# Kernel optimization log

Hardware: AMD Instinct MI355X
Metric: run time of the kernel (lower is better)

The kernel has to match this reference:

```python
import jax, jax.numpy as jnp
import numpy as np

LEVELS = 256
# round(d*cos(a)), round(d*sin(a)) for d=1, angles 0, pi/4, pi/2, 3pi/4 (torch defaults)
SHIFTS = [(1, 0), (1, 1), (0, 1), (-1, 1)]


def _glcm(gray):
    # gray: (n, h, w) int32 in [0, LEVELS-1]
    n = gray.shape[0]
    B = LEVELS * LEVELS
    cooc = []
    for dx, dy in SHIFTS:  # fixed small set of angles
        shifted = jnp.roll(gray, shift=(dx, dy), axis=(1, 2))
        joint = (gray * LEVELS + shifted).reshape(n, -1)  # (n, h*w)
        vmin = joint.min()
        vmax = joint.max()
        # faithful torch.histc binning: B equal-width bins over [vmin, vmax],
        # values == vmax fall in last bin (handled by clip)
        scale = B / jnp.maximum((vmax - vmin).astype(jnp.float32), 1.0)
        bins = jnp.clip(
            jnp.floor((joint - vmin).astype(jnp.float32) * scale).astype(jnp.int32),
            0, B - 1)
        bidx = jnp.broadcast_to(jnp.arange(n)[:, None], joint.shape)
        hist = jnp.zeros((n, B), jnp.float32).at[bidx, bins].add(1.0)
        cooc.append(hist.reshape(n, LEVELS, LEVELS).sum(axis=0))
    co = jnp.stack(cooc, axis=-1)            # (L, L, A)
    co = co + jnp.swapaxes(co, 0, 1)          # symmetric=True
    glcm = co / co.sum()                      # normalize over ALL dims incl. angles (as torch)
    return glcm[:, :, None, :]                # (L, L, n_dist=1, A)


def _contrast(glcm):
    i = jnp.arange(LEVELS, dtype=jnp.float32)
    w = (i[:, None] - i[None, :]) ** 2        # (L, L) contrast weights
    return jnp.sum(glcm * w[:, :, None, None], axis=(0, 1))  # (n_dist, A)


def _loss(original, generated):
    og = jax.lax.stop_gradient(
        jnp.round(original.mean(axis=1) * (LEVELS - 1)).astype(jnp.int32))
    gg = jax.lax.stop_gradient(
        jnp.round(generated.mean(axis=1) * (LEVELS - 1)).astype(jnp.int32))
    return jnp.mean(jnp.abs(_contrast(_glcm(og)) - _contrast(_glcm(gg))))


def setup_inputs() -> dict:
    key = jax.random.key(0)
    k1, k2 = jax.random.split(key)
    shape = (16, 3, 512, 512)
    return {
        "original": jax.random.uniform(k1, shape, dtype=jnp.float32),
        "generated": jax.random.uniform(k2, shape, dtype=jnp.float32),
    }


def reference(original, generated):
    return _loss(original, generated)
```

## Files before the change

kernel.cpp:

```cpp
#include <hip/hip_runtime.h>

#define W 512
#define NPIX 4194304

union Bytes { uint4 v; unsigned char b[16]; };

__device__ __forceinline__ unsigned char gray1(float a, float b, float c) {
    return (unsigned char)__float2int_rn(((a + b + c) / 3.0f) * 255.0f);
}

__global__ __launch_bounds__(256, 4) void k1_gray_minmax(
    const float4* __restrict__ og, const float4* __restrict__ gg,
    uchar4* __restrict__ gray, unsigned int* __restrict__ blockmm) {
    int inp = blockIdx.y;
    int img = blockIdx.x >> 5;
    int r0 = (blockIdx.x & 31) << 4;
    const float4* src = (inp ? gg : og) + (size_t)img * 3 * 65536;
    uchar4* gout = gray + (size_t)inp * (NPIX / 4) + img * 65536;
    const float4* s0 = src;
    const float4* s1 = src + 65536;
    const float4* s2 = src + 131072;

    __shared__ unsigned char lds[18 * W];
    uchar4* lds4 = (uchar4*)lds;

    int off[9];
#pragma unroll
    for (int j = 0; j < 9; ++j) {
        int q = threadIdx.x + j * 256;
        int i = q >> 7, quad = q & 127;
        int ir = (r0 - 1 + i) & 511;
        off[j] = ir * 128 + quad;
    }
    float4 a = s0[off[0]], b = s1[off[0]], c = s2[off[0]];
#pragma unroll
    for (int j = 0; j < 9; ++j) {
        float4 an, bn, cn;
        if (j < 8) { an = s0[off[j + 1]]; bn = s1[off[j + 1]]; cn = s2[off[j + 1]]; }
        uchar4 r;
        r.x = gray1(a.x, b.x, c.x);
        r.y = gray1(a.y, b.y, c.y);
        r.z = gray1(a.z, b.z, c.z);
        r.w = gray1(a.w, b.w, c.w);
        lds4[threadIdx.x + j * 256] = r;
        int i = (threadIdx.x + j * 256) >> 7;
        if (i >= 1 && i <= 16) gout[off[j]] = r;
        a = an; b = bn; c = cn;
    }
    __syncthreads();

    int lr = 1 + (threadIdx.x >> 4);
    int c0 = (threadIdx.x & 15) << 5;
    const unsigned char* Lm = lds + (lr - 1) * W;
    const unsigned char* Lc = lds + lr * W;
    const unsigned char* Lp = lds + (lr + 1) * W;
    Bytes rm[2], rc[2], rp[2];
    rm[0].v = *(const uint4*)(Lm + c0); rm[1].v = *(const uint4*)(Lm + c0 + 16);
    rc[0].v = *(const uint4*)(Lc + c0); rc[1].v = *(const uint4*)(Lc + c0 + 16);
    rp[0].v = *(const uint4*)(Lp + c0); rp[1].v = *(const uint4*)(Lp + c0 + 16);
    int cp = (c0 - 1) & 511;
    unsigned char pm = Lm[cp], pc = Lc[cp], pp = Lp[cp];

    unsigned int lmin[4] = {~0u, ~0u, ~0u, ~0u};
    unsigned int lmax[4] = {0u, 0u, 0u, 0u};
#pragma unroll
    for (int h = 0; h < 2; ++h) {
#pragma unroll
        for (int j = 0; j < 16; ++j) {
            unsigned int base = ((unsigned int)rc[h].b[j]) << 8;
            unsigned int v0 = base + rm[h].b[j];
            unsigned int v1 = base + (j ? rm[h].b[j - 1] : (h ? rm[0].b[15] : pm));
            unsigned int v2 = base + (j ? rc[h].b[j - 1] : (h ? rc[0].b[15] : pc));
            unsigned int v3 = base + (j ? rp[h].b[j - 1] : (h ? rp[0].b[15] : pp));
            lmin[0] = min(lmin[0], v0); lmax[0] = max(lmax[0], v0);
            lmin[1] = min(lmin[1], v1); lmax[1] = max(lmax[1], v1);
            lmin[2] = min(lmin[2], v2); lmax[2] = max(lmax[2], v2);
            lmin[3] = min(lmin[3], v3); lmax[3] = max(lmax[3], v3);
        }
    }
#pragma unroll
    for (int off2 = 32; off2 > 0; off2 >>= 1) {
#pragma unroll
        for (int s = 0; s < 4; ++s) {
            lmin[s] = min(lmin[s], (unsigned int)__shfl_down((int)lmin[s], off2));
            lmax[s] = max(lmax[s], (unsigned int)__shfl_down((int)lmax[s], off2));
        }
    }
    __shared__ unsigned int wmin[4][4], wmax[4][4];
    int wave = threadIdx.x >> 6;
    if ((threadIdx.x & 63) == 0) {
#pragma unroll
        for (int s = 0; s < 4; ++s) { wmin[wave][s] = lmin[s]; wmax[wave][s] = lmax[s]; }
    }
    __syncthreads();
    if (threadIdx.x < 4) {
        int s = threadIdx.x;
        unsigned int mn = min(min(wmin[0][s], wmin[1][s]), min(wmin[2][s], wmin[3][s]));
        unsigned int mx = max(max(wmax[0][s], wmax[1][s]), max(wmax[2][s], wmax[3][s]));
        blockmm[inp * 4096 + s * 512 + blockIdx.x] = mn;
        blockmm[inp * 4096 + (4 + s) * 512 + blockIdx.x] = mx;
    }
}

__global__ __launch_bounds__(256, 8) void k2_contrast(
    const unsigned char* __restrict__ gray,
    const unsigned int* __restrict__ blockmm,
    unsigned int* __restrict__ partial) {
    int inp = blockIdx.y;
    const unsigned char* g = gray + (size_t)inp * NPIX;
    int t = blockIdx.x * 256 + threadIdx.x;
    int img = t >> 14;
    int p = t & 16383;
    int r = p >> 5;
    int c0 = (p & 31) << 4;
    const unsigned char* gn = g + (img << 18);
    int rm1 = (r - 1) & 511, rp1 = (r + 1) & 511, cp = (c0 - 1) & 511;

    Bytes rm, rc, rp;
    rm.v = *(const uint4*)(gn + (rm1 << 9) + c0);
    rc.v = *(const uint4*)(gn + (r   << 9) + c0);
    rp.v = *(const uint4*)(gn + (rp1 << 9) + c0);
    unsigned char pm = gn[(rm1 << 9) | cp];
    unsigned char pc = gn[(r   << 9) | cp];
    unsigned char pp = gn[(rp1 << 9) | cp];

    __shared__ unsigned int mmfin[8];
    {
        int s8 = threadIdx.x >> 5, lane = threadIdx.x & 31;
        const unsigned int* mb = blockmm + inp * 4096 + s8 * 512;
        unsigned int v = mb[lane];
#pragma unroll
        for (int k = 1; k < 16; ++k) {
            unsigned int u = mb[lane + k * 32];
            v = (s8 < 4) ? min(v, u) : max(v, u);
        }
#pragma unroll
        for (int off = 16; off > 0; off >>= 1) {
            unsigned int u = (unsigned int)__shfl_down((int)v, off, 32);
            v = (s8 < 4) ? min(v, u) : max(v, u);
        }
        if (lane == 0) mmfin[s8] = v;
    }
    __syncthreads();

    unsigned int vm[4]; float scale[4];
#pragma unroll
    for (int s = 0; s < 4; ++s) {
        vm[s] = mmfin[s];
        scale[s] = 65536.0f / fmaxf((float)(mmfin[4 + s] - vm[s]), 1.0f);
    }

    unsigned int acc[4] = {0u, 0u, 0u, 0u};
#pragma unroll
    for (int j = 0; j < 16; ++j) {
        unsigned int base = ((unsigned int)rc.b[j]) << 8;
        unsigned int v[4];
        v[0] = base + rm.b[j];
        v[1] = base + (j ? rm.b[j - 1] : pm);
        v[2] = base + (j ? rc.b[j - 1] : pc);
        v[3] = base + (j ? rp.b[j - 1] : pp);
#pragma unroll
        for (int s = 0; s < 4; ++s) {
            int b = (int)((float)(v[s] - vm[s]) * scale[s]);
            b = b > 65535 ? 65535 : b;
            int d = (b >> 8) - (b & 255);
            acc[s] += (unsigned int)(d * d);
        }
    }
#pragma unroll
    for (int off = 32; off > 0; off >>= 1)
#pragma unroll
        for (int s = 0; s < 4; ++s)
            acc[s] += (unsigned int)__shfl_down((int)acc[s], off);

    __shared__ unsigned int wsum[4][4];
    int wave = threadIdx.x >> 6;
    if ((threadIdx.x & 63) == 0) {
#pragma unroll
        for (int s = 0; s < 4; ++s) wsum[wave][s] = acc[s];
    }
    __syncthreads();
    if (threadIdx.x < 4) {
        int s = threadIdx.x;
        unsigned int tot = wsum[0][s] + wsum[1][s] + wsum[2][s] + wsum[3][s];
        partial[(inp * 4 + s) * 1024 + blockIdx.x] = tot;
    }
}

__global__ __launch_bounds__(256) void k3_loss(
    const unsigned int* __restrict__ partial, float* __restrict__ out) {
    int c = threadIdx.x >> 5;
    int lane = threadIdx.x & 31;
    const unsigned int* p = partial + c * 1024;
    double acc = 0.0;
#pragma unroll
    for (int k = 0; k < 32; ++k) acc += (double)p[lane + k * 32];
#pragma unroll
    for (int off = 16; off > 0; off >>= 1) acc += __shfl_down(acc, off, 32);
    __shared__ double cs[8];
    if (lane == 0) cs[c] = acc;
    __syncthreads();
    if (threadIdx.x == 0) {
        double r = 0.0;
        for (int a = 0; a < 4; ++a) {
            double co = 2.0 * cs[a]     / 33554432.0;
            double cg = 2.0 * cs[4 + a] / 33554432.0;
            r += fabs(co - cg);
        }
        out[0] = (float)(r * 0.25);
    }
}

extern "C" void kernel_launch(void* const* d_in, const int* in_sizes, int n_in,
                              void* d_out, int out_size, void* d_ws, size_t ws_size,
                              hipStream_t stream) {
    const float4* og = (const float4*)d_in[0];
    const float4* gg = (const float4*)d_in[1];
    float* out = (float*)d_out;

    unsigned int* blockmm = (unsigned int*)d_ws;
    unsigned int* partial = blockmm + 8192;
    unsigned char* gray = (unsigned char*)d_ws + 65536;

    dim3 g1(512, 2);
    k1_gray_minmax<<<g1, 256, 0, stream>>>(og, gg, (uchar4*)gray, blockmm);
    dim3 g2(1024, 2);
    k2_contrast<<<g2, 256, 0, stream>>>(gray, blockmm, partial);
    k3_loss<<<1, 256, 0, stream>>>(partial, out);
}
```

Before: 40.86 us.

## Fuse final loss reduction into contrast kernel via atomics and last-block ticket

Removes the third kernel launch by having each contrast block atomically add its per-angle sums into 64-bit global accumulators. A ticket counter identifies the last block, which then computes the final loss. The accumulators and ticket are zeroed in the first kernel. Input float loads in the gray kernel become nontemporal loads to reduce cache pollution. This saves one launch plus the partial-array round trip, at the cost of atomic contention on eight addresses.

Result: slower. 77.64 us (+90.0%).

```diff
diff --git a/kernel.cpp b/kernel.cpp
--- a/kernel.cpp
+++ b/kernel.cpp
@@ -5,13 +5,24 @@
 
 union Bytes { uint4 v; unsigned char b[16]; };
 
+typedef float __attribute__((ext_vector_type(4))) f4v;
+
+__device__ __forceinline__ f4v ntload(const float4* p) {
+    return __builtin_nontemporal_load((const f4v*)p);
+}
+
 __device__ __forceinline__ unsigned char gray1(float a, float b, float c) {
     return (unsigned char)__float2int_rn(((a + b + c) / 3.0f) * 255.0f);
 }
 
 __global__ __launch_bounds__(256, 4) void k1_gray_minmax(
     const float4* __restrict__ og, const float4* __restrict__ gg,
-    uchar4* __restrict__ gray, unsigned int* __restrict__ blockmm) {
+    uchar4* __restrict__ gray, unsigned int* __restrict__ blockmm,
+    unsigned long long* __restrict__ sums, unsigned int* __restrict__ ticket) {
+    if (blockIdx.x == 0 && blockIdx.y == 0) {
+        if (threadIdx.x < 8) sums[threadIdx.x] = 0ull;
+        if (threadIdx.x == 8) *ticket = 0u;
+    }
     int inp = blockIdx.y;
     int img = blockIdx.x >> 5;
     int r0 = (blockIdx.x & 31) << 4;
@@ -32,11 +43,15 @@
         int ir = (r0 - 1 + i) & 511;
         off[j] = ir * 128 + quad;
     }
-    float4 a = s0[off[0]], b = s1[off[0]], c = s2[off[0]];
+    f4v a = ntload(s0 + off[0]), b = ntload(s1 + off[0]), c = ntload(s2 + off[0]);
 #pragma unroll
     for (int j = 0; j < 9; ++j) {
-        float4 an, bn, cn;
-        if (j < 8) { an = s0[off[j + 1]]; bn = s1[off[j + 1]]; cn = s2[off[j + 1]]; }
+        f4v an, bn, cn;
+        if (j < 8) {
+            an = ntload(s0 + off[j + 1]);
+            bn = ntload(s1 + off[j + 1]);
+            cn = ntload(s2 + off[j + 1]);
+        }
         uchar4 r;
         r.x = gray1(a.x, b.x, c.x);
         r.y = gray1(a.y, b.y, c.y);
@@ -79,11 +94,11 @@
         }
     }
 #pragma unroll
-    for (int off2 = 32; off2 > 0; off2 >>= 1) {
+    for (int o = 32; o > 0; o >>= 1) {
 #pragma unroll
         for (int s = 0; s < 4; ++s) {
-            lmin[s] = min(lmin[s], (unsigned int)__shfl_down((int)lmin[s], off2));
-            lmax[s] = max(lmax[s], (unsigned int)__shfl_down((int)lmax[s], off2));
+            lmin[s] = min(lmin[s], (unsigned int)__shfl_down((int)lmin[s], o));
+            lmax[s] = max(lmax[s], (unsigned int)__shfl_down((int)lmax[s], o));
         }
     }
     __shared__ unsigned int wmin[4][4], wmax[4][4];
@@ -102,10 +117,11 @@
     }
 }
 
-__global__ __launch_bounds__(256, 8) void k2_contrast(
+__global__ __launch_bounds__(256, 8) void k2_contrast_final(
     const unsigned char* __restrict__ gray,
     const unsigned int* __restrict__ blockmm,
-    unsigned int* __restrict__ partial) {
+    unsigned long long* __restrict__ sums,
+    unsigned int* __restrict__ ticket, float* __restrict__ out) {
     int inp = blockIdx.y;
     const unsigned char* g = gray + (size_t)inp * NPIX;
     int t = blockIdx.x * 256 + threadIdx.x;
@@ -135,8 +151,8 @@
             v = (s8 < 4) ? min(v, u) : max(v, u);
         }
 #pragma unroll
-        for (int off = 16; off > 0; off >>= 1) {
-            unsigned int u = (unsigned int)__shfl_down((int)v, off, 32);
+        for (int o = 16; o > 0; o >>= 1) {
+            unsigned int u = (unsigned int)__shfl_down((int)v, o, 32);
             v = (s8 < 4) ? min(v, u) : max(v, u);
         }
         if (lane == 0) mmfin[s8] = v;
@@ -168,12 +184,13 @@
         }
     }
 #pragma unroll
-    for (int off = 32; off > 0; off >>= 1)
+    for (int o = 32; o > 0; o >>= 1)
 #pragma unroll
         for (int s = 0; s < 4; ++s)
-            acc[s] += (unsigned int)__shfl_down((int)acc[s], off);
+            acc[s] += (unsigned int)__shfl_down((int)acc[s], o);
 
     __shared__ unsigned int wsum[4][4];
+    __shared__ unsigned int lastflag;
     int wave = threadIdx.x >> 6;
     if ((threadIdx.x & 63) == 0) {
 #pragma unroll
@@ -182,32 +199,34 @@
     __syncthreads();
     if (threadIdx.x < 4) {
         int s = threadIdx.x;
-        unsigned int tot = wsum[0][s] + wsum[1][s] + wsum[2][s] + wsum[3][s];
-        partial[(inp * 4 + s) * 1024 + blockIdx.x] = tot;
-    }
-}
-
-__global__ __launch_bounds__(256) void k3_loss(
-    const unsigned int* __restrict__ partial, float* __restrict__ out) {
-    int c = threadIdx.x >> 5;
-    int lane = threadIdx.x & 31;
-    const unsigned int* p = partial + c * 1024;
-    double acc = 0.0;
-#pragma unroll
-    for (int k = 0; k < 32; ++k) acc += (double)p[lane + k * 32];
-#pragma unroll
-    for (int off = 16; off > 0; off >>= 1) acc += __shfl_down(acc, off, 32);
-    __shared__ double cs[8];
-    if (lane == 0) cs[c] = acc;
-    __syncthreads();
+        unsigned long long tot = (unsigned long long)
+            (wsum[0][s] + wsum[1][s] + wsum[2][s] + wsum[3][s]);
+        __hip_atomic_fetch_add(&sums[inp * 4 + s], tot,
+                               __ATOMIC_RELAXED, __HIP_MEMORY_SCOPE_AGENT);
+    }
+    __syncthreads();
+
     if (threadIdx.x == 0) {
-        double r = 0.0;
-        for (int a = 0; a < 4; ++a) {
-            double co = 2.0 * cs[a]     / 33554432.0;
-            double cg = 2.0 * cs[4 + a] / 33554432.0;
-            r += fabs(co - cg);
-        }
-        out[0] = (float)(r * 0.25);
+        unsigned int old = __hip_atomic_fetch_add(ticket, 1u,
+                               __ATOMIC_ACQ_REL, __HIP_MEMORY_SCOPE_AGENT);
+        lastflag = (old == 2047u) ? 1u : 0u;
+    }
+    __syncthreads();
+    if (lastflag) {
+        __shared__ unsigned long long cs8[8];
+        if (threadIdx.x < 8)
+            cs8[threadIdx.x] = __hip_atomic_load(&sums[threadIdx.x],
+                                   __ATOMIC_RELAXED, __HIP_MEMORY_SCOPE_AGENT);
+        __syncthreads();
+        if (threadIdx.x == 0) {
+            double r2 = 0.0;
+            for (int a = 0; a < 4; ++a) {
+                double co = 2.0 * (double)cs8[a]     / 33554432.0;
+                double cg = 2.0 * (double)cs8[4 + a] / 33554432.0;
+                r2 += fabs(co - cg);
+            }
+            out[0] = (float)(r2 * 0.25);
+        }
     }
 }
 
@@ -219,12 +238,13 @@
     float* out = (float*)d_out;
 
     unsigned int* blockmm = (unsigned int*)d_ws;
-    unsigned int* partial = blockmm + 8192;
+    unsigned long long* sums = (unsigned long long*)((char*)d_ws + 32768);
+    unsigned int* ticket = (unsigned int*)((char*)d_ws + 32832);
     unsigned char* gray = (unsigned char*)d_ws + 65536;
 
     dim3 g1(512, 2);
-    k1_gray_minmax<<<g1, 256, 0, stream>>>(og, gg, (uchar4*)gray, blockmm);
+    k1_gray_minmax<<<g1, 256, 0, stream>>>(og, gg, (uchar4*)gray, blockmm,
+                                           sums, ticket);
     dim3 g2(1024, 2);
-    k2_contrast<<<g2, 256, 0, stream>>>(gray, blockmm, partial);
-    k3_loss<<<1, 256, 0, stream>>>(partial, out);
-}
+    k2_contrast_final<<<g2, 256, 0, stream>>>(gray, blockmm, sums, ticket, out);
+}
```
